# Kernel tuning notes

Hardware: AMD Instinct MI355X
Metric: run time of the kernel (lower is better)

The kernel has to match this reference:

```python
import jax, jax.numpy as jnp
import numpy as np

N_HEAD = 16


def setup_inputs() -> dict:
    key = jax.random.key(0)
    k0, k1, k2, k3 = jax.random.split(key, 4)
    B, T, C = 2, 2048, 1024
    scale = 0.02
    x = jax.random.normal(k0, (B, T, C), dtype=jnp.float32)
    W_attn = jax.random.normal(k1, (C, 3 * C), dtype=jnp.float32) * scale
    b_attn = jnp.zeros((3 * C,), dtype=jnp.float32)
    W_proj = jax.random.normal(k2, (C, C), dtype=jnp.float32) * scale
    b_proj = jnp.zeros((C,), dtype=jnp.float32)
    return {"x": x, "W_attn": W_attn, "b_attn": b_attn, "W_proj": W_proj, "b_proj": b_proj}


def reference(x, W_attn, b_attn, W_proj, b_proj):
    B, T, C = x.shape
    H = N_HEAD
    hd = C // H
    # fused qkv projection
    qkv = x @ W_attn + b_attn                      # [B, T, 3C]
    q, k, v = jnp.split(qkv, 3, axis=-1)
    q = q.reshape(B, T, H, hd).transpose(0, 2, 1, 3)  # [B, H, T, hd]
    k = k.reshape(B, T, H, hd).transpose(0, 2, 1, 3)
    v = v.reshape(B, T, H, hd).transpose(0, 2, 1, 3)
    # scaled dot-product attention with causal mask (past_kv=None -> seq_len == T)
    att = jnp.einsum('bhqd,bhkd->bhqk', q, k) / jnp.sqrt(jnp.float32(hd))
    causal = jnp.tril(jnp.ones((T, T), dtype=bool))  # [T, T]
    att = jnp.where(causal[None, None, :, :], att, jnp.float32(-jnp.inf))
    att = jax.nn.softmax(att, axis=-1)
    y = jnp.einsum('bhqk,bhkd->bhqd', att, v)        # [B, H, T, hd]
    y = y.transpose(0, 2, 1, 3).reshape(B, T, C)
    y = y @ W_proj + b_proj
    return (y, k, v)  # (output, present_k, present_v)
```

## Files before the change

kernel.cpp:

```cpp
#include <hip/hip_runtime.h>
#include <hip/hip_bf16.h>

typedef __bf16 bf16;
typedef __bf16 bf16x8 __attribute__((ext_vector_type(8)));
typedef float f32x4 __attribute__((ext_vector_type(4)));
typedef unsigned int u32;

#define MFMA_BF16(a, b, c) __builtin_amdgcn_mfma_f32_16x16x32_bf16((a), (b), (c), 0, 0, 0)

#define SEQ_T 2048
#define DIM_C 1024

__device__ inline void gload16(const void* g, void* l) {
  __builtin_amdgcn_global_load_lds((const __attribute__((address_space(1))) u32*)g,
                                   (__attribute__((address_space(3))) u32*)l, 16, 0, 0);
}

__global__ __launch_bounds__(256) void prep_kernel(
    const float* __restrict__ x, const float* __restrict__ Wa,
    const float* __restrict__ Wp, bf16* __restrict__ xbf,
    bf16* __restrict__ wat, bf16* __restrict__ wpt) {
  const int tid = threadIdx.x;
  const int bid = blockIdx.x;
  if (bid < 2048) {
    const size_t i = ((size_t)bid * 256 + tid) * 8;
    const f32x4 a = *(const f32x4*)(x + i);
    const f32x4 b = *(const f32x4*)(x + i + 4);
    bf16x8 r;
    r[0] = (bf16)a[0]; r[1] = (bf16)a[1]; r[2] = (bf16)a[2]; r[3] = (bf16)a[3];
    r[4] = (bf16)b[0]; r[5] = (bf16)b[1]; r[6] = (bf16)b[2]; r[7] = (bf16)b[3];
    *(bf16x8*)(xbf + i) = r;
  } else if (bid < 3584) {
    const int cid = (bid - 2048) * 256 + tid;
    const int kg = cid / 3072, n = cid - kg * 3072;
    bf16x8 r;
#pragma unroll
    for (int j = 0; j < 8; j++) r[j] = (bf16)Wa[(size_t)(kg * 8 + j) * 3072 + n];
    *(bf16x8*)(wat + (size_t)cid * 8) = r;
  } else {
    const int cid = (bid - 3584) * 256 + tid;
    const int kg = cid >> 10, n = cid & 1023;
    bf16x8 r;
#pragma unroll
    for (int j = 0; j < 8; j++) r[j] = (bf16)Wp[(size_t)(kg * 8 + j) * 1024 + n];
    *(bf16x8*)(wpt + (size_t)cid * 8) = r;
  }
}

template <int MODE, int BM>
__global__ __launch_bounds__(256) void gemm_kernel(
    const bf16* __restrict__ A, const bf16* __restrict__ Wt,
    const float* __restrict__ bias, float* __restrict__ out0,
    float* __restrict__ out1, bf16* __restrict__ bq, bf16* __restrict__ bk2,
    int M, int N, int K) {
  constexpr int MI = BM / 32;
  constexpr int CA = BM / 64;
  __shared__ bf16 As[2][BM * 32];
  __shared__ bf16 Bt[2][128 * 32];

  const int tid = threadIdx.x;
  const int wid = tid >> 6, lane = tid & 63;
  const int quad = lane >> 4, l16 = lane & 15;
  const int wm = (wid >> 1) * (BM / 2), wn = (wid & 1) * 64;
  const int m0 = blockIdx.y * BM, n0 = blockIdx.x * 128;
  const int lr = lane >> 2, lks = lane & 3;

  const f32x4 zero = {0.f, 0.f, 0.f, 0.f};
  f32x4 acc[MI][4];
#pragma unroll
  for (int i = 0; i < MI; i++)
#pragma unroll
    for (int j = 0; j < 4; j++) acc[i][j] = zero;

  auto stage = [&](int buf, int kk) {
#pragma unroll
    for (int p = 0; p < CA; p++) {
      const int c = wid * CA + p;
      gload16(A + (size_t)(m0 + c * 16 + lr) * K + kk + lks * 8,
              (bf16*)As[buf] + c * 512);
    }
#pragma unroll
    for (int p = 0; p < 2; p++) {
      const int c = wid * 2 + p;
      gload16(Wt + ((size_t)((kk >> 3) + lks) * N + n0 + c * 16 + lr) * 8,
              (bf16*)Bt[buf] + c * 512);
    }
  };

  const int nt = K >> 5;
  stage(0, 0);
  __syncthreads();
  int cur = 0;
  for (int t = 0; t < nt; t++) {
    if (t + 1 < nt) stage(cur ^ 1, (t + 1) << 5);
    bf16x8 af[MI], bfr[4];
#pragma unroll
    for (int i = 0; i < MI; i++)
      af[i] = *(const bf16x8*)&As[cur][(wm + i * 16 + l16) * 32 + quad * 8];
#pragma unroll
    for (int j = 0; j < 4; j++)
      bfr[j] = *(const bf16x8*)&Bt[cur][(wn + j * 16 + l16) * 32 + quad * 8];
#pragma unroll
    for (int i = 0; i < MI; i++)
#pragma unroll
      for (int j = 0; j < 4; j++)
        acc[i][j] = MFMA_BF16(af[i], bfr[j], acc[i][j]);
    __syncthreads();
    cur ^= 1;
  }

#pragma unroll
  for (int i = 0; i < MI; i++) {
#pragma unroll
    for (int j = 0; j < 4; j++) {
      const int col = n0 + wn + j * 16 + l16;
      const float bv = bias[col];
#pragma unroll
      for (int r = 0; r < 4; r++) {
        const int gm = m0 + wm + i * 16 + quad * 4 + r;
        const float v = acc[i][j][r] + bv;
        if (MODE == 0) {
          out0[(size_t)gm * N + col] = v;
        } else {
          const int which = col >> 10, c = col & 1023;
          const int h = c >> 6, d = c & 63;
          const int b = gm >> 11, t = gm & (SEQ_T - 1);
          const size_t idx = ((size_t)(b * 16 + h) * SEQ_T + t) * 64 + d;
          if (which == 0) {
            bq[idx] = (bf16)(v * 0.18033688f);
          } else if (which == 1) {
            out0[idx] = v;
            bk2[idx] = (bf16)v;
          } else {
            out1[idx] = v;
          }
        }
      }
    }
  }
}

__global__ __launch_bounds__(512) void attn_kernel(
    const bf16* __restrict__ Qbf, const bf16* __restrict__ Kbf,
    const float* __restrict__ V, bf16* __restrict__ Y) {
  __shared__ bf16 Ks[2][64 * 72];
  __shared__ bf16 Vt[2][64 * 72];
  __shared__ bf16 Ps[8 * 16 * 72];

  const int tid = threadIdx.x;
  const int wid = tid >> 6, lane = tid & 63;
  const int quad = lane >> 4, l16 = lane & 15;

  const int qt = (blockIdx.y < 16) ? ((int)gridDim.x - 1 - (int)blockIdx.x)
                                   : (int)blockIdx.x;
  const int bh = blockIdx.y;
  const int q0 = qt * 128;
  const int b = bh >> 4, h = bh & 15;

  const bf16* qp = Qbf + (size_t)bh * SEQ_T * 64;
  const bf16* kp = Kbf + (size_t)bh * SEQ_T * 64;
  const float* vp = V + (size_t)bh * SEQ_T * 64;

  bf16x8 aq[2];
#pragma unroll
  for (int ks = 0; ks < 2; ks++)
    aq[ks] = *(const bf16x8*)(qp + (size_t)(q0 + wid * 16 + l16) * 64 + ks * 32 + quad * 8);

  bf16x8 bones;
#pragma unroll
  for (int j = 0; j < 8; j++) bones[j] = (bf16)1.0f;

  const f32x4 zero = {0.f, 0.f, 0.f, 0.f};
  f32x4 oacc[4], lacc;
  lacc = zero;
#pragma unroll
  for (int t = 0; t < 4; t++) oacc[t] = zero;

  const int last = 2 * qt + 1;
  bf16x8 kreg;
  f32x4 vf[2];

  auto load_tile = [&](int t) {
    const size_t base = (size_t)t * 64 * 64;
    kreg = *(const bf16x8*)(kp + base + (size_t)tid * 8);
    vf[0] = *(const f32x4*)(vp + base + (size_t)tid * 8);
    vf[1] = *(const f32x4*)(vp + base + (size_t)tid * 8 + 4);
  };
  auto stage_tile = [&](int buf) {
    const int key = tid >> 3, hs = tid & 7;
    *(bf16x8*)&Ks[buf][key * 72 + hs * 8] = kreg;
#pragma unroll
    for (int e = 0; e < 8; e++) {
      const float v = (e < 4) ? vf[0][e] : vf[1][e - 4];
      const int hr = hs * 8 + e;
      Vt[buf][hr * 72 + (((key >> 3) ^ hs) * 8) + (key & 7)] = (bf16)v;
    }
  };

  load_tile(0);
  stage_tile(0);
  load_tile(1);

  for (int it = 0; it <= last; ++it) {
    const int cur = it & 1;
    __syncthreads();
    if (it < last) stage_tile(cur ^ 1);
    if (it + 1 < last) load_tile(it + 2);

    const bool skip = (it == last) && (wid < 4);
    const bool dm = (it == 2 * qt && wid < 4) || (it == last && wid >= 4);

    f32x4 sa[4];
    if (!skip) {
      __builtin_amdgcn_s_setprio(1);
#pragma unroll
      for (int nt = 0; nt < 4; nt++) {
        const bf16x8 bk0 = *(const bf16x8*)&Ks[cur][(nt * 16 + l16) * 72 + quad * 8];
        const bf16x8 bk1 = *(const bf16x8*)&Ks[cur][(nt * 16 + l16) * 72 + 32 + quad * 8];
        f32x4 s = MFMA_BF16(aq[0], bk0, zero);
        sa[nt] = MFMA_BF16(aq[1], bk1, s);
      }
      __builtin_amdgcn_s_setprio(0);
      if (dm) {
#pragma unroll
        for (int nt = 0; nt < 4; nt++) {
          const int col = it * 64 + nt * 16 + l16;
#pragma unroll
          for (int r = 0; r < 4; r++) {
            const int row = q0 + wid * 16 + quad * 4 + r;
            if (col > row) sa[nt][r] = -1e30f;
          }
        }
      }
      bf16* pwb = &Ps[wid * 16 * 72];
#pragma unroll
      for (int nt = 0; nt < 4; nt++) {
        const int cb = nt * 16 + l16;
#pragma unroll
        for (int r = 0; r < 4; r++) {
          const int pr = quad * 4 + r;
          pwb[pr * 72 + (((cb >> 3) ^ (pr & 7)) * 8) + (cb & 7)] = (bf16)exp2f(sa[nt][r]);
        }
      }
      bf16x8 ap[2];
#pragma unroll
      for (int ks = 0; ks < 2; ks++)
        ap[ks] = *(const bf16x8*)&pwb[l16 * 72 + (((ks * 4 + quad) ^ (l16 & 7)) * 8)];
      __builtin_amdgcn_s_setprio(1);
      lacc = MFMA_BF16(ap[0], bones, lacc);
      lacc = MFMA_BF16(ap[1], bones, lacc);
#pragma unroll
      for (int nt = 0; nt < 4; nt++) {
        const int n = nt * 16 + l16;
#pragma unroll
        for (int ks = 0; ks < 2; ks++) {
          const bf16x8 bv = *(const bf16x8*)&Vt[cur][n * 72 + (((ks * 4 + quad) ^ (n >> 3)) * 8)];
          oacc[nt] = MFMA_BF16(ap[ks], bv, oacc[nt]);
        }
      }
      __builtin_amdgcn_s_setprio(0);
    }
  }

  float inv[4];
#pragma unroll
  for (int r = 0; r < 4; r++) inv[r] = 1.f / lacc[r];
#pragma unroll
  for (int nt = 0; nt < 4; nt++) {
#pragma unroll
    for (int r = 0; r < 4; r++) {
      const int row = q0 + wid * 16 + quad * 4 + r;
      const int col = h * 64 + nt * 16 + l16;
      Y[((size_t)(b * SEQ_T + row)) * DIM_C + col] = (bf16)(oacc[nt][r] * inv[r]);
    }
  }
}

extern "C" void kernel_launch(void* const* d_in, const int* in_sizes, int n_in,
                              void* d_out, int out_size, void* d_ws, size_t ws_size,
                              hipStream_t stream) {
  (void)in_sizes; (void)n_in; (void)out_size; (void)ws_size;
  const float* x = (const float*)d_in[0];
  const float* W_attn = (const float*)d_in[1];
  const float* b_attn = (const float*)d_in[2];
  const float* W_proj = (const float*)d_in[3];
  const float* b_proj = (const float*)d_in[4];

  float* out = (float*)d_out;
  float* y_out = out;
  float* k_out = out + (size_t)4194304;
  float* v_out = out + (size_t)8388608;
  bf16* qbf = (bf16*)d_out;
  bf16* kbf = (bf16*)d_out + 4194304;
  bf16* y_att = (bf16*)d_in[0];
  bf16* xbf = (bf16*)d_ws;
  bf16* wat = xbf + 4194304;
  bf16* wpt = wat + 3145728;

  prep_kernel<<<4096, 256, 0, stream>>>(x, W_attn, W_proj, xbf, wat, wpt);
  gemm_kernel<1, 128><<<dim3(3072 / 128, 4096 / 128), 256, 0, stream>>>(
      xbf, wat, b_attn, k_out, v_out, qbf, kbf, 4096, 3072, 1024);
  attn_kernel<<<dim3(SEQ_T / 128, 32), 512, 0, stream>>>(qbf, kbf, v_out, y_att);
  gemm_kernel<0, 64><<<dim3(1024 / 128, 4096 / 64), 256, 0, stream>>>(
      y_att, wpt, b_proj, y_out, nullptr, nullptr, nullptr, 4096, 1024, 1024);
}
```

Baseline: 200.9 us.

## Pre-swizzle bf16 K/V tiles and stream them to LDS via global_load_lds

A new kernel converts the fp32 K and V outputs into bf16 tile images whose layout already matches the attention kernel's swizzled LDS layout, with V stored transposed. The attention kernel can then stage each tile with direct global-to-LDS loads instead of register round-trips, per-element transposed LDS stores and fp32 conversion. The QKV GEMM no longer writes a bf16 K copy, and the output projection GEMM now uses BK=64. The s_setprio hints are removed. The cost is an extra kernel launch and an extra read of K/V in fp32.

```diff
diff --git a/kernel.cpp b/kernel.cpp
--- a/kernel.cpp
+++ b/kernel.cpp
@@ -14,6 +14,13 @@
 __device__ inline void gload16(const void* g, void* l) {
   __builtin_amdgcn_global_load_lds((const __attribute__((address_space(1))) u32*)g,
                                    (__attribute__((address_space(3))) u32*)l, 16, 0, 0);
+}
+
+__device__ inline bf16x8 cvt8f(const f32x4 a, const f32x4 b) {
+  bf16x8 r;
+  r[0] = (bf16)a[0]; r[1] = (bf16)a[1]; r[2] = (bf16)a[2]; r[3] = (bf16)a[3];
+  r[4] = (bf16)b[0]; r[5] = (bf16)b[1]; r[6] = (bf16)b[2]; r[7] = (bf16)b[3];
+  return r;
 }
 
 __global__ __launch_bounds__(256) void prep_kernel(
@@ -24,12 +31,7 @@
   const int bid = blockIdx.x;
   if (bid < 2048) {
     const size_t i = ((size_t)bid * 256 + tid) * 8;
-    const f32x4 a = *(const f32x4*)(x + i);
-    const f32x4 b = *(const f32x4*)(x + i + 4);
-    bf16x8 r;
-    r[0] = (bf16)a[0]; r[1] = (bf16)a[1]; r[2] = (bf16)a[2]; r[3] = (bf16)a[3];
-    r[4] = (bf16)b[0]; r[5] = (bf16)b[1]; r[6] = (bf16)b[2]; r[7] = (bf16)b[3];
-    *(bf16x8*)(xbf + i) = r;
+    *(bf16x8*)(xbf + i) = cvt8f(*(const f32x4*)(x + i), *(const f32x4*)(x + i + 4));
   } else if (bid < 3584) {
     const int cid = (bid - 2048) * 256 + tid;
     const int kg = cid / 3072, n = cid - kg * 3072;
@@ -47,23 +49,43 @@
   }
 }
 
-template <int MODE, int BM>
+__global__ __launch_bounds__(256) void img_kernel(
+    const float* __restrict__ K, const float* __restrict__ V,
+    bf16* __restrict__ kimg, bf16* __restrict__ vimg) {
+  const int gid = blockIdx.x * 256 + threadIdx.x;
+  const int ka = gid >> 3, h8 = gid & 7;
+  const size_t src = (size_t)ka * 64 + h8 * 8;
+  const bf16x8 rk = cvt8f(*(const f32x4*)(K + src), *(const f32x4*)(K + src + 4));
+  const bf16x8 rv = cvt8f(*(const f32x4*)(V + src), *(const f32x4*)(V + src + 4));
+  const size_t tb = (size_t)(ka & ~63) * 64;
+  const int kl = ka & 63, k7 = ka & 7, cq = (ka >> 3) & 7;
+  *(bf16x8*)(kimg + tb + kl * 64 + ((h8 ^ k7) * 8)) = rk;
+#pragma unroll
+  for (int e = 0; e < 8; e++) {
+    const int hr = h8 * 8 + e;
+    vimg[tb + hr * 64 + ((cq ^ (hr & 7)) * 8) + k7] = rv[e];
+  }
+}
+
+template <int MODE, int BM, int BK>
 __global__ __launch_bounds__(256) void gemm_kernel(
     const bf16* __restrict__ A, const bf16* __restrict__ Wt,
     const float* __restrict__ bias, float* __restrict__ out0,
-    float* __restrict__ out1, bf16* __restrict__ bq, bf16* __restrict__ bk2,
-    int M, int N, int K) {
+    float* __restrict__ out1, bf16* __restrict__ bq, int M, int N, int K) {
   constexpr int MI = BM / 32;
-  constexpr int CA = BM / 64;
-  __shared__ bf16 As[2][BM * 32];
-  __shared__ bf16 Bt[2][128 * 32];
+  constexpr int CA = BM * BK / 2048;
+  constexpr int CB = BK / 16;
+  constexpr int RPC = 512 / BK;
+  constexpr int EPB = BK / 8;
+  __shared__ bf16 As[2][BM * BK];
+  __shared__ bf16 Bt[2][128 * BK];
 
   const int tid = threadIdx.x;
   const int wid = tid >> 6, lane = tid & 63;
   const int quad = lane >> 4, l16 = lane & 15;
   const int wm = (wid >> 1) * (BM / 2), wn = (wid & 1) * 64;
   const int m0 = blockIdx.y * BM, n0 = blockIdx.x * 128;
-  const int lr = lane >> 2, lks = lane & 3;
+  const int lr = lane / EPB, lks = lane % EPB;
 
   const f32x4 zero = {0.f, 0.f, 0.f, 0.f};
   f32x4 acc[MI][4];
@@ -76,35 +98,38 @@
 #pragma unroll
     for (int p = 0; p < CA; p++) {
       const int c = wid * CA + p;
-      gload16(A + (size_t)(m0 + c * 16 + lr) * K + kk + lks * 8,
+      gload16(A + (size_t)(m0 + c * RPC + lr) * K + kk + lks * 8,
               (bf16*)As[buf] + c * 512);
     }
 #pragma unroll
-    for (int p = 0; p < 2; p++) {
-      const int c = wid * 2 + p;
-      gload16(Wt + ((size_t)((kk >> 3) + lks) * N + n0 + c * 16 + lr) * 8,
+    for (int p = 0; p < CB; p++) {
+      const int c = wid * CB + p;
+      gload16(Wt + ((size_t)((kk >> 3) + lks) * N + n0 + c * RPC + lr) * 8,
               (bf16*)Bt[buf] + c * 512);
     }
   };
 
-  const int nt = K >> 5;
+  const int nt = K / BK;
   stage(0, 0);
   __syncthreads();
   int cur = 0;
   for (int t = 0; t < nt; t++) {
-    if (t + 1 < nt) stage(cur ^ 1, (t + 1) << 5);
-    bf16x8 af[MI], bfr[4];
-#pragma unroll
-    for (int i = 0; i < MI; i++)
-      af[i] = *(const bf16x8*)&As[cur][(wm + i * 16 + l16) * 32 + quad * 8];
-#pragma unroll
-    for (int j = 0; j < 4; j++)
-      bfr[j] = *(const bf16x8*)&Bt[cur][(wn + j * 16 + l16) * 32 + quad * 8];
-#pragma unroll
-    for (int i = 0; i < MI; i++)
+    if (t + 1 < nt) stage(cur ^ 1, (t + 1) * BK);
+#pragma unroll
+    for (int kb = 0; kb < BK / 32; kb++) {
+      bf16x8 af[MI], bfr[4];
+#pragma unroll
+      for (int i = 0; i < MI; i++)
+        af[i] = *(const bf16x8*)&As[cur][(wm + i * 16 + l16) * BK + kb * 32 + quad * 8];
 #pragma unroll
       for (int j = 0; j < 4; j++)
-        acc[i][j] = MFMA_BF16(af[i], bfr[j], acc[i][j]);
+        bfr[j] = *(const bf16x8*)&Bt[cur][(wn + j * 16 + l16) * BK + kb * 32 + quad * 8];
+#pragma unroll
+      for (int i = 0; i < MI; i++)
+#pragma unroll
+        for (int j = 0; j < 4; j++)
+          acc[i][j] = MFMA_BF16(af[i], bfr[j], acc[i][j]);
+    }
     __syncthreads();
     cur ^= 1;
   }
@@ -130,7 +155,6 @@
             bq[idx] = (bf16)(v * 0.18033688f);
           } else if (which == 1) {
             out0[idx] = v;
-            bk2[idx] = (bf16)v;
           } else {
             out1[idx] = v;
           }
@@ -141,11 +165,11 @@
 }
 
 __global__ __launch_bounds__(512) void attn_kernel(
-    const bf16* __restrict__ Qbf, const bf16* __restrict__ Kbf,
-    const float* __restrict__ V, bf16* __restrict__ Y) {
-  __shared__ bf16 Ks[2][64 * 72];
-  __shared__ bf16 Vt[2][64 * 72];
-  __shared__ bf16 Ps[8 * 16 * 72];
+    const bf16* __restrict__ Qbf, const bf16* __restrict__ Kimg,
+    const bf16* __restrict__ Vimg, bf16* __restrict__ Y) {
+  __shared__ bf16 Ks[2][4096];
+  __shared__ bf16 Vt[2][4096];
+  __shared__ bf16 Ps[8 * 1024];
 
   const int tid = threadIdx.x;
   const int wid = tid >> 6, lane = tid & 63;
@@ -158,8 +182,8 @@
   const int b = bh >> 4, h = bh & 15;
 
   const bf16* qp = Qbf + (size_t)bh * SEQ_T * 64;
-  const bf16* kp = Kbf + (size_t)bh * SEQ_T * 64;
-  const float* vp = V + (size_t)bh * SEQ_T * 64;
+  const bf16* kp = Kimg + (size_t)bh * SEQ_T * 64;
+  const bf16* vp = Vimg + (size_t)bh * SEQ_T * 64;
 
   bf16x8 aq[2];
 #pragma unroll
@@ -177,50 +201,34 @@
   for (int t = 0; t < 4; t++) oacc[t] = zero;
 
   const int last = 2 * qt + 1;
-  bf16x8 kreg;
-  f32x4 vf[2];
-
-  auto load_tile = [&](int t) {
-    const size_t base = (size_t)t * 64 * 64;
-    kreg = *(const bf16x8*)(kp + base + (size_t)tid * 8);
-    vf[0] = *(const f32x4*)(vp + base + (size_t)tid * 8);
-    vf[1] = *(const f32x4*)(vp + base + (size_t)tid * 8 + 4);
+
+  auto stage = [&](int buf, int t) {
+    const size_t tb = (size_t)t * 4096 + (size_t)tid * 8;
+    bf16* wb = &Ks[buf][wid << 9];
+    gload16(kp + tb, wb);
+    gload16(vp + tb, &Vt[buf][wid << 9]);
   };
-  auto stage_tile = [&](int buf) {
-    const int key = tid >> 3, hs = tid & 7;
-    *(bf16x8*)&Ks[buf][key * 72 + hs * 8] = kreg;
-#pragma unroll
-    for (int e = 0; e < 8; e++) {
-      const float v = (e < 4) ? vf[0][e] : vf[1][e - 4];
-      const int hr = hs * 8 + e;
-      Vt[buf][hr * 72 + (((key >> 3) ^ hs) * 8) + (key & 7)] = (bf16)v;
-    }
-  };
-
-  load_tile(0);
-  stage_tile(0);
-  load_tile(1);
+
+  stage(0, 0);
+  __syncthreads();
 
   for (int it = 0; it <= last; ++it) {
     const int cur = it & 1;
-    __syncthreads();
-    if (it < last) stage_tile(cur ^ 1);
-    if (it + 1 < last) load_tile(it + 2);
+    if (it < last) stage(cur ^ 1, it + 1);
 
     const bool skip = (it == last) && (wid < 4);
     const bool dm = (it == 2 * qt && wid < 4) || (it == last && wid >= 4);
 
-    f32x4 sa[4];
     if (!skip) {
-      __builtin_amdgcn_s_setprio(1);
+      f32x4 sa[4];
 #pragma unroll
       for (int nt = 0; nt < 4; nt++) {
-        const bf16x8 bk0 = *(const bf16x8*)&Ks[cur][(nt * 16 + l16) * 72 + quad * 8];
-        const bf16x8 bk1 = *(const bf16x8*)&Ks[cur][(nt * 16 + l16) * 72 + 32 + quad * 8];
+        const int row = nt * 16 + l16, r7 = l16 & 7;
+        const bf16x8 bk0 = *(const bf16x8*)&Ks[cur][row * 64 + ((quad ^ r7) * 8)];
+        const bf16x8 bk1 = *(const bf16x8*)&Ks[cur][row * 64 + (((quad + 4) ^ r7) * 8)];
         f32x4 s = MFMA_BF16(aq[0], bk0, zero);
         sa[nt] = MFMA_BF16(aq[1], bk1, s);
       }
-      __builtin_amdgcn_s_setprio(0);
       if (dm) {
 #pragma unroll
         for (int nt = 0; nt < 4; nt++) {
@@ -232,34 +240,33 @@
           }
         }
       }
-      bf16* pwb = &Ps[wid * 16 * 72];
+      bf16* pwb = &Ps[wid * 1024];
 #pragma unroll
       for (int nt = 0; nt < 4; nt++) {
-        const int cb = nt * 16 + l16;
 #pragma unroll
         for (int r = 0; r < 4; r++) {
           const int pr = quad * 4 + r;
-          pwb[pr * 72 + (((cb >> 3) ^ (pr & 7)) * 8) + (cb & 7)] = (bf16)exp2f(sa[nt][r]);
+          pwb[pr * 64 + (((2 * nt + (l16 >> 3)) ^ (pr & 7)) * 8) + (l16 & 7)] =
+              (bf16)exp2f(sa[nt][r]);
         }
       }
       bf16x8 ap[2];
 #pragma unroll
       for (int ks = 0; ks < 2; ks++)
-        ap[ks] = *(const bf16x8*)&pwb[l16 * 72 + (((ks * 4 + quad) ^ (l16 & 7)) * 8)];
-      __builtin_amdgcn_s_setprio(1);
+        ap[ks] = *(const bf16x8*)&pwb[l16 * 64 + (((ks * 4 + quad) ^ (l16 & 7)) * 8)];
       lacc = MFMA_BF16(ap[0], bones, lacc);
       lacc = MFMA_BF16(ap[1], bones, lacc);
 #pragma unroll
       for (int nt = 0; nt < 4; nt++) {
-        const int n = nt * 16 + l16;
+        const int hr = nt * 16 + l16, h7 = l16 & 7;
 #pragma unroll
         for (int ks = 0; ks < 2; ks++) {
-          const bf16x8 bv = *(const bf16x8*)&Vt[cur][n * 72 + (((ks * 4 + quad) ^ (n >> 3)) * 8)];
+          const bf16x8 bv = *(const bf16x8*)&Vt[cur][hr * 64 + (((ks * 4 + quad) ^ h7) * 8)];
           oacc[nt] = MFMA_BF16(ap[ks], bv, oacc[nt]);
         }
       }
-      __builtin_amdgcn_s_setprio(0);
-    }
+    }
+    __syncthreads();
   }
 
   float inv[4];
@@ -291,16 +298,18 @@
   float* k_out = out + (size_t)4194304;
   float* v_out = out + (size_t)8388608;
   bf16* qbf = (bf16*)d_out;
-  bf16* kbf = (bf16*)d_out + 4194304;
+  bf16* kimg = (bf16*)d_out + 4194304;
   bf16* y_att = (bf16*)d_in[0];
+  bf16* vimg = (bf16*)d_in[0] + 4194304;
   bf16* xbf = (bf16*)d_ws;
   bf16* wat = xbf + 4194304;
   bf16* wpt = wat + 3145728;
 
   prep_kernel<<<4096, 256, 0, stream>>>(x, W_attn, W_proj, xbf, wat, wpt);
-  gemm_kernel<1, 128><<<dim3(3072 / 128, 4096 / 128), 256, 0, stream>>>(
-      xbf, wat, b_attn, k_out, v_out, qbf, kbf, 4096, 3072, 1024);
-  attn_kernel<<<dim3(SEQ_T / 128, 32), 512, 0, stream>>>(qbf, kbf, v_out, y_att);
-  gemm_kernel<0, 64><<<dim3(1024 / 128, 4096 / 64), 256, 0, stream>>>(
-      y_att, wpt, b_proj, y_out, nullptr, nullptr, nullptr, 4096, 1024, 1024);
-}
+  gemm_kernel<1, 128, 32><<<dim3(3072 / 128, 4096 / 128), 256, 0, stream>>>(
+      xbf, wat, b_attn, k_out, v_out, qbf, 4096, 3072, 1024);
+  img_kernel<<<2048, 256, 0, stream>>>(k_out, v_out, kimg, vimg);
+  attn_kernel<<<dim3(SEQ_T / 128, 32), 512, 0, stream>>>(qbf, kimg, vimg, y_att);
+  gemm_kernel<0, 64, 64><<<dim3(1024 / 128, 4096 / 64), 256, 0, stream>>>(
+      y_att, wpt, b_proj, y_out, nullptr, nullptr, 4096, 1024, 1024);
+}
```

Result: slower. 207.2 us (+3.2%).
